# Kernel optimization log

Hardware: AMD Instinct MI355X
Metric: run time of the kernel (lower is better)

The kernel has to match this reference:

```python
import jax, jax.numpy as jnp
import numpy as np

N = 20000      # nodes
E = 640000     # edges (before self loops)
IN = 256       # in_channels == out_channels (forced by classifier size 4*in)
H1, C1 = 8, 16   # conv1: heads=8, out=16 -> concat 128
H2, C2 = 1, 256  # conv2: heads=1, out=out_channels
B = 4096       # article pairs
NEG_SLOPE = 0.2  # PyG GATv2Conv default negative_slope


def setup_inputs() -> dict:
    key = jax.random.key(0)
    ks = jax.random.split(key, 24)
    s = 0.05
    inp = {
        "gnn_x": jax.random.normal(ks[0], (N, IN), jnp.float32),
        "vanilla_x": jax.random.normal(ks[1], (N, IN), jnp.float32),
        "edge_src": jax.random.randint(ks[2], (E,), 0, N, jnp.int32),
        "edge_dst": jax.random.randint(ks[3], (E,), 0, N, jnp.int32),
        "a1_idx": jax.random.randint(ks[4], (B,), 0, N, jnp.int64),
        "a2_idx": jax.random.randint(ks[5], (B,), 0, N, jnp.int64),
        # conv1 params (lin_l, lin_r, att, bias)
        "Wl1": jax.random.normal(ks[6], (IN, H1 * C1), jnp.float32) * s,
        "bl1": jnp.zeros((H1 * C1,), jnp.float32),
        "Wr1": jax.random.normal(ks[7], (IN, H1 * C1), jnp.float32) * s,
        "br1": jnp.zeros((H1 * C1,), jnp.float32),
        "att1": jax.random.normal(ks[8], (H1, C1), jnp.float32) * s,
        "bias1": jnp.zeros((H1 * C1,), jnp.float32),
        # conv2 params
        "Wl2": jax.random.normal(ks[9], (H1 * C1, H2 * C2), jnp.float32) * s,
        "bl2": jnp.zeros((H2 * C2,), jnp.float32),
        "Wr2": jax.random.normal(ks[10], (H1 * C1, H2 * C2), jnp.float32) * s,
        "br2": jnp.zeros((H2 * C2,), jnp.float32),
        "att2": jax.random.normal(ks[11], (H2, C2), jnp.float32) * s,
        "bias2": jnp.zeros((H2 * C2,), jnp.float32),
        # classifier
        "Wc": jax.random.normal(ks[12], (4 * IN, 1), jnp.float32) * s,
        "bc": jnp.zeros((1,), jnp.float32),
    }
    return inp


def _gatv2_layer(x, src, dst, Wl, bl, Wr, br, att, bias):
    """GATv2Conv: x_l = lin_l(x)[src], x_r = lin_r(x)[dst];
    e = att . leaky_relu(x_l + x_r); segment softmax over dst; scatter-add x_l*alpha."""
    n = x.shape[0]
    h, c = att.shape
    xl = (x @ Wl + bl).reshape(n, h, c)
    xr = (x @ Wr + br).reshape(n, h, c)
    # per-edge attention logits [E, H]
    e = jnp.einsum('ehc,hc->eh', jax.nn.leaky_relu(xl[src] + xr[dst], NEG_SLOPE), att)
    # segment softmax over destination nodes (self loops guarantee non-empty segments)
    emax = jax.ops.segment_max(e, dst, num_segments=n)
    ex = jnp.exp(e - emax[dst])
    denom = jax.ops.segment_sum(ex, dst, num_segments=n)
    alpha = ex / denom[dst]                      # [E, H]
    out = jax.ops.segment_sum(alpha[:, :, None] * xl[src], dst, num_segments=n)  # [N,H,C]
    return out.reshape(n, h * c) + bias          # concat=True (heads=1 identical)


def reference(gnn_x, vanilla_x, Wl1, bl1, Wr1, br1, att1, bias1,
              Wl2, bl2, Wr2, br2, att2, bias2, Wc, bc,
              edge_src, edge_dst, a1_idx, a2_idx):
    n = gnn_x.shape[0]
    loops = jnp.arange(n, dtype=edge_src.dtype)
    src = jnp.concatenate([edge_src, loops])     # PyG add_self_loops=True
    dst = jnp.concatenate([edge_dst, loops])
    x = _gatv2_layer(gnn_x, src, dst, Wl1, bl1, Wr1, br1, att1, bias1)
    x = jax.nn.relu(x)
    x = _gatv2_layer(x, src, dst, Wl2, bl2, Wr2, br2, att2, bias2)
    combined = jnp.concatenate(
        [vanilla_x[a1_idx], vanilla_x[a2_idx], x[a1_idx], x[a2_idx]], axis=1)  # [B, 4*IN]
    logits = combined @ Wc + bc                  # [B, 1]
    return logits
```

## Files before the change

### kernel.cpp

```cpp
#include <hip/hip_runtime.h>
#include <math.h>

#define N_NODES 20000
#define M_PAD   20032
#define E_EDGES 640000
#define ET (E_EDGES + N_NODES)
#define IN_CH 256
#define D1 128
#define D2 256
#define BPAIRS 4096
#define NEG 0.2f
#define LOG2E 1.4426950408889634f

#define ZC_BLOCKS    40
#define WT_BLOCKS    32
#define XCONV_BLOCKS (M_PAD * IN_CH / 4 / 4 / 256)
#define PREP_BLOCKS  (ZC_BLOCKS + WT_BLOCKS + XCONV_BLOCKS)

#define COUNT_BLOCKS ((ET + 255) / 256)
#define SCAT_BLOCKS  ((ET + 255) / 256)
#define G1X (M_PAD / 64)
#define G1_BLOCKS (G1X * (D1 / 64))
#define K2_GEMM0 (1 + COUNT_BLOCKS)
#define K2_SCAT0 (K2_GEMM0 + G1_BLOCKS)
#define K2_BLOCKS (K2_SCAT0 + SCAT_BLOCKS)

#if __has_builtin(__builtin_amdgcn_exp2f)
#define EXP2F(x) __builtin_amdgcn_exp2f(x)
#else
#define EXP2F(x) exp2f(x)
#endif

typedef __bf16 bf16x8 __attribute__((ext_vector_type(8)));
typedef float  f32x4  __attribute__((ext_vector_type(4)));
typedef float  f32x2  __attribute__((ext_vector_type(2)));
typedef unsigned short u16x4 __attribute__((ext_vector_type(4)));

__device__ __forceinline__ unsigned short f2b(float f) {
    unsigned int u = __float_as_uint(f);
    unsigned int r = u + 0x7FFFu + ((u >> 16) & 1u);
    return (unsigned short)(r >> 16);
}
__device__ __forceinline__ unsigned char f2f8(float f) {
    return (unsigned char)(__builtin_amdgcn_cvt_pk_fp8_f32(f, f, 0, false) & 0xFF);
}
template <bool HI>
__device__ __forceinline__ f32x2 f8up2(unsigned int u) {
    return __builtin_amdgcn_cvt_pk_f32_fp8((int)u, HI);
}
__device__ __forceinline__ f32x2 up2(unsigned int u) {
    f32x2 r;
    r.x = __uint_as_float(u << 16);
    r.y = __uint_as_float(u & 0xFFFF0000u);
    return r;
}
__device__ __forceinline__ f32x2 lrelu2(f32x2 s) {
    return __builtin_elementwise_max(s, s * NEG);
}
__device__ __forceinline__ float lrelu(float s) { return fmaxf(s, NEG * s); }

__device__ __forceinline__ void unpack8(uint4 u, float* v) {
    v[0] = __uint_as_float(u.x << 16); v[1] = __uint_as_float(u.x & 0xFFFF0000u);
    v[2] = __uint_as_float(u.y << 16); v[3] = __uint_as_float(u.y & 0xFFFF0000u);
    v[4] = __uint_as_float(u.z << 16); v[5] = __uint_as_float(u.z & 0xFFFF0000u);
    v[6] = __uint_as_float(u.w << 16); v[7] = __uint_as_float(u.w & 0xFFFF0000u);
}
__device__ __forceinline__ void unpack8_f8(uint2 u, float* v) {
    f32x2 a = f8up2<false>(u.x), b = f8up2<true>(u.x);
    f32x2 c = f8up2<false>(u.y), d = f8up2<true>(u.y);
    v[0] = a.x; v[1] = a.y; v[2] = b.x; v[3] = b.y;
    v[4] = c.x; v[5] = c.y; v[6] = d.x; v[7] = d.y;
}

__device__ __forceinline__ int aload(const int* p) {
    return __hip_atomic_load(p, __ATOMIC_RELAXED, __HIP_MEMORY_SCOPE_AGENT);
}


__global__ __launch_bounds__(256) void prep_kernel(
        const float* __restrict__ gnn_x,
        const float* __restrict__ Wl1, const float* __restrict__ Wr1,
        const float* __restrict__ Wl2, const float* __restrict__ Wr2,
        unsigned short* __restrict__ xb,
        unsigned short* __restrict__ wt1l, unsigned short* __restrict__ wt1r,
        unsigned short* __restrict__ wt2l, unsigned short* __restrict__ wt2r,
        int* __restrict__ ibuf) {
    __shared__ __align__(16) unsigned short tile[64 * 65];
    int bid = blockIdx.x;
    if (bid < ZC_BLOCKS) {
        int q = bid * 256 + threadIdx.x;
        int4 z; z.x = z.y = z.z = z.w = 0;
        ((int4*)ibuf)[q] = z;
    } else if (bid < ZC_BLOCKS + WT_BLOCKS) {
        int t = bid - ZC_BLOCKS;
        int m = t >> 3;
        int tt = t & 7;
        const float* W;
        unsigned short* Wt;
        int K, N;
        if (m == 0)      { W = Wl1; Wt = wt1l; K = IN_CH; N = D1; }
        else if (m == 1) { W = Wr1; Wt = wt1r; K = IN_CH; N = D1; }
        else if (m == 2) { W = Wl2; Wt = wt2l; K = D1; N = D2; }
        else             { W = Wr2; Wt = wt2r; K = D1; N = D2; }
        int ntn = N >> 6;
        int k0 = (tt / ntn) << 6;
        int n0 = (tt % ntn) << 6;
        int c = threadIdx.x & 63;
        int rr = threadIdx.x >> 6;
#pragma unroll
        for (int ch = 0; ch < 16; ch++) {
            int row = rr * 16 + ch;
            tile[row * 65 + c] = f2b(W[(size_t)(k0 + row) * N + n0 + c]);
        }
        __syncthreads();
#pragma unroll
        for (int ch = 0; ch < 16; ch++) {
            int n = rr * 16 + ch;
            Wt[(size_t)(n0 + n) * K + k0 + c] = tile[c * 65 + n];
        }
    } else {
        int tid = (bid - ZC_BLOCKS - WT_BLOCKS) * 256 + threadIdx.x;
        const int NQ = M_PAD * IN_CH / 4;
        int q0 = tid * 4;
#pragma unroll
        for (int j = 0; j < 4; j++) {
            int qi = q0 + j;
            if (qi >= NQ) break;
            int e0 = qi * 4;
            int row = e0 >> 8;
            u16x4 o;
            if (row < N_NODES) {
                f32x4 v = __builtin_nontemporal_load((const f32x4*)(gnn_x + e0));
                o.x = f2b(v.x); o.y = f2b(v.y); o.z = f2b(v.z); o.w = f2b(v.w);
            } else {
                o.x = o.y = o.z = o.w = 0;
            }
            *(u16x4*)(xb + e0) = o;
        }
    }
}

__device__ __forceinline__ void scan256(const int* __restrict__ count,
                                        int* __restrict__ offsets,
                                        int* wbuf) {
    const int PER = 79;
    int t = threadIdx.x;
    int base = t * PER;
    int sum = 0;
#pragma unroll 8
    for (int i = 0; i < PER; i++) {
        int idx = base + i;
        if (idx < N_NODES) sum += count[idx];
    }
    int lane = t & 63, wave = t >> 6;
    int s = sum;
#pragma unroll
    for (int off = 1; off < 64; off <<= 1) {
        int x = __shfl_up(s, off);
        if (lane >= off) s += x;
    }
    int* wsum = wbuf;
    int* wpre = wbuf + 4;
    if (lane == 63) wsum[wave] = s;
    __syncthreads();
    if (t == 0) {
        int acc = 0;
        for (int w = 0; w < 4; w++) { wpre[w] = acc; acc += wsum[w]; }
    }
    __syncthreads();
    int excl = wpre[wave] + (s - sum);
    if (t == 255) offsets[N_NODES] = excl + sum;
    int run = excl;
#pragma unroll 8
    for (int i = 0; i < PER; i++) {
        int idx = base + i;
        if (idx < N_NODES) { offsets[idx] = run; run += count[idx]; }
    }
}

template <int K>
__device__ __forceinline__ void dual_gemm_tile(
        const unsigned short* __restrict__ A,
        const unsigned short* __restrict__ Wtl,
        const unsigned short* __restrict__ Wtr,
        const float* __restrict__ bl, const float* __restrict__ br,
        unsigned char* __restrict__ Yl, unsigned short* __restrict__ Yr,
        int M, int NOUT, int bx, int by) {
    const int NK = K / 32;
    int wave = threadIdx.x >> 6;
    int lane = threadIdx.x & 63;
    int row0 = bx * 64;
    int col0 = (by * 4 + wave) * 16;
    int rsub = lane & 15;
    int koff = (lane >> 4) * 8;

    const unsigned short* ap  = A   + (size_t)(row0 + rsub) * K + koff;
    const unsigned short* bpl = Wtl + (size_t)(col0 + rsub) * K + koff;
    const unsigned short* bpr = Wtr + (size_t)(col0 + rsub) * K + koff;

    f32x4 l0 = {0.f, 0.f, 0.f, 0.f};
    f32x4 l1 = l0, l2 = l0, l3 = l0, r0 = l0, r1 = l0, r2 = l0, r3 = l0;

#pragma unroll
    for (int kb = 0; kb < NK; kb++) {
        int off = kb * 32;
        bf16x8 bfl = *(const bf16x8*)(bpl + off);
        bf16x8 bfr = *(const bf16x8*)(bpr + off);
        bf16x8 a0 = *(const bf16x8*)(ap + off);
        bf16x8 a1 = *(const bf16x8*)(ap + 16 * K + off);
        bf16x8 a2 = *(const bf16x8*)(ap + 32 * K + off);
        bf16x8 a3 = *(const bf16x8*)(ap + 48 * K + off);
        l0 = __builtin_amdgcn_mfma_f32_16x16x32_bf16(a0, bfl, l0, 0, 0, 0);
        r0 = __builtin_amdgcn_mfma_f32_16x16x32_bf16(a0, bfr, r0, 0, 0, 0);
        l1 = __builtin_amdgcn_mfma_f32_16x16x32_bf16(a1, bfl, l1, 0, 0, 0);
        r1 = __builtin_amdgcn_mfma_f32_16x16x32_bf16(a1, bfr, r1, 0, 0, 0);
        l2 = __builtin_amdgcn_mfma_f32_16x16x32_bf16(a2, bfl, l2, 0, 0, 0);
        r2 = __builtin_amdgcn_mfma_f32_16x16x32_bf16(a2, bfr, r2, 0, 0, 0);
        l3 = __builtin_amdgcn_mfma_f32_16x16x32_bf16(a3, bfl, l3, 0, 0, 0);
        r3 = __builtin_amdgcn_mfma_f32_16x16x32_bf16(a3, bfr, r3, 0, 0, 0);
    }

    int colg = col0 + rsub;
    float bvl = bl[colg];
    float bvr = br[colg];
    int rbase = row0 + (lane >> 4) * 4;
#pragma unroll
    for (int t = 0; t < 4; t++) {
        f32x4 al = (t == 0) ? l0 : (t == 1) ? l1 : (t == 2) ? l2 : l3;
        f32x4 ar = (t == 0) ? r0 : (t == 1) ? r1 : (t == 2) ? r2 : r3;
#pragma unroll
        for (int r = 0; r < 4; r++) {
            int row = rbase + t * 16 + r;
            if (row < M) {
                Yl[(size_t)row * NOUT + colg] = f2f8(al[r] + bvl);
                Yr[(size_t)row * NOUT + colg] = f2b(ar[r] + bvr);
            }
        }
    }
}


__global__ __launch_bounds__(256) void sort_gemm1_kernel(
        const int* __restrict__ edge_src, const int* __restrict__ edge_dst,
        int* __restrict__ count, int* __restrict__ cursor,
        int* __restrict__ done, int* __restrict__ flag,
        int* __restrict__ offsets, int* __restrict__ sorted_src,
        const unsigned short* __restrict__ A,
        const unsigned short* __restrict__ Wtl,
        const unsigned short* __restrict__ Wtr,
        const float* __restrict__ bl, const float* __restrict__ br,
        unsigned char* __restrict__ Yl, unsigned short* __restrict__ Yr) {
    __shared__ int wbuf[8];
    int bid = blockIdx.x, tid = threadIdx.x;
    if (bid == 0) {
        if (tid == 0) {
            int guard = 0;
            while (aload(done) < COUNT_BLOCKS && guard < (1 << 30)) {
                __builtin_amdgcn_s_sleep(8); guard++;
            }
        }
        __syncthreads();
        scan256(count, offsets, wbuf);
        __builtin_amdgcn_s_waitcnt(0);
        __syncthreads();
        if (tid == 0)
            __hip_atomic_store(flag, 1, __ATOMIC_RELEASE,
                               __HIP_MEMORY_SCOPE_AGENT);
    } else if (bid <= COUNT_BLOCKS) {
        int e = (bid - 1) * 256 + tid;
        if (e < ET) {
            int dst = (e < E_EDGES) ? edge_dst[e] : (e - E_EDGES);
            atomicAdd(&count[dst], 1);
        }
        __builtin_amdgcn_s_waitcnt(0);
        __syncthreads();
        if (tid == 0)
            __hip_atomic_fetch_add(done, 1, __ATOMIC_RELAXED,
                                   __HIP_MEMORY_SCOPE_AGENT);
    } else if (bid < K2_SCAT0) {
        int t = bid - K2_GEMM0;
        dual_gemm_tile<IN_CH>(A, Wtl, Wtr, bl, br, Yl, Yr,
                              N_NODES, D1, t % G1X, t / G1X);
    } else {
        if (tid == 0) {
            int guard = 0;
            while (aload(flag) == 0 && guard < (1 << 30)) {
                __builtin_amdgcn_s_sleep(8); guard++;
            }
        }
        __syncthreads();
        int e = (bid - K2_SCAT0) * 256 + tid;
        if (e < ET) {
            int dst = (e < E_EDGES) ? edge_dst[e] : (e - E_EDGES);
            int src = (e < E_EDGES) ? edge_src[e] : (e - E_EDGES);
            sorted_src[offsets[dst] + atomicAdd(&cursor[dst], 1)] = src;
        }
    }
}


__global__ __launch_bounds__(256) void aggregate1_kernel(
        const unsigned char* __restrict__ xl1, const unsigned short* __restrict__ xr1,
        const float* __restrict__ att1, const float* __restrict__ bias1,
        const int* __restrict__ offsets, const int* __restrict__ sorted_src,
        unsigned short* __restrict__ x1) {
    int wave = threadIdx.x >> 6;
    int lane = threadIdx.x & 63;
    int q = lane >> 4;
    int ql = lane & 15;
    int dst = blockIdx.x * 4 + wave;
    if (dst >= M_PAD) return;
    int c0 = ql * 8;
    if (dst >= N_NODES) {
        if (q == 0) {
            uint4 z; z.x = z.y = z.z = z.w = 0;
            *(uint4*)(x1 + (size_t)dst * D1 + c0) = z;
        }
        return;
    }

    uint4 xu = *(const uint4*)(xr1 + (size_t)dst * D1 + c0);
    f32x2 xr[4] = {up2(xu.x), up2(xu.y), up2(xu.z), up2(xu.w)};
    float4 aa0 = *(const float4*)(att1 + c0);
    float4 aa1 = *(const float4*)(att1 + c0 + 4);
    f32x2 att[4];
    att[0].x = aa0.x * LOG2E; att[0].y = aa0.y * LOG2E;
    att[1].x = aa0.z * LOG2E; att[1].y = aa0.w * LOG2E;
    att[2].x = aa1.x * LOG2E; att[2].y = aa1.y * LOG2E;
    att[3].x = aa1.z * LOG2E; att[3].y = aa1.w * LOG2E;

    int beg = offsets[dst], end = offsets[dst + 1];
    const unsigned char* base = xl1 + c0;

    float l = 0.f;
    f32x2 acc[4] = {{0.f,0.f},{0.f,0.f},{0.f,0.f},{0.f,0.f}};

    int i = beg;
    int s0 = sorted_src[min(i + q, end - 1)];
    uint2 g0 = *(const uint2*)(base + (size_t)s0 * D1);
    bool more1 = (i + 4) < end;
    uint2 g1;
    if (more1) {
        int s1 = sorted_src[min(i + 4 + q, end - 1)];
        g1 = *(const uint2*)(base + (size_t)s1 * D1);
    }
    while (true) {
        bool more2 = (i + 8) < end;
        uint2 g2;
        if (more2) {
            int s2 = sorted_src[min(i + 8 + q, end - 1)];
            g2 = *(const uint2*)(base + (size_t)s2 * D1);
        }
        bool act = (i + q) < end;
        f32x2 v0 = f8up2<false>(g0.x), v1 = f8up2<true>(g0.x);
        f32x2 v2 = f8up2<false>(g0.y), v3 = f8up2<true>(g0.y);
        f32x2 p2 = att[0] * lrelu2(v0 + xr[0]);
        p2 += att[1] * lrelu2(v1 + xr[1]);
        p2 += att[2] * lrelu2(v2 + xr[2]);
        p2 += att[3] * lrelu2(v3 + xr[3]);
        float p = p2.x + p2.y;
        p += __shfl_xor(p, 1);
        float w = act ? EXP2F(p) : 0.f;
        l += w;
        acc[0] += w * v0; acc[1] += w * v1; acc[2] += w * v2; acc[3] += w * v3;
        if (!more1) break;
        i += 4;
        g0 = g1; g1 = g2; more1 = more2;
    }
    l += __shfl_xor(l, 16);
    l += __shfl_xor(l, 32);
#pragma unroll
    for (int j = 0; j < 4; j++) {
        f32x2 t;
        t.x = __shfl_xor(acc[j].x, 16); t.y = __shfl_xor(acc[j].y, 16);
        acc[j] += t;
        t.x = __shfl_xor(acc[j].x, 32); t.y = __shfl_xor(acc[j].y, 32);
        acc[j] += t;
    }
    if (q == 0) {
        float inv = 1.f / l;
        float4 bb0 = *(const float4*)(bias1 + c0);
        float4 bb1 = *(const float4*)(bias1 + c0 + 4);
        unsigned short o[8];
        o[0] = f2b(fmaxf(acc[0].x * inv + bb0.x, 0.f));
        o[1] = f2b(fmaxf(acc[0].y * inv + bb0.y, 0.f));
        o[2] = f2b(fmaxf(acc[1].x * inv + bb0.z, 0.f));
        o[3] = f2b(fmaxf(acc[1].y * inv + bb0.w, 0.f));
        o[4] = f2b(fmaxf(acc[2].x * inv + bb1.x, 0.f));
        o[5] = f2b(fmaxf(acc[2].y * inv + bb1.y, 0.f));
        o[6] = f2b(fmaxf(acc[3].x * inv + bb1.z, 0.f));
        o[7] = f2b(fmaxf(acc[3].y * inv + bb1.w, 0.f));
        uint4 ov;
        ov.x = (unsigned int)o[0] | ((unsigned int)o[1] << 16);
        ov.y = (unsigned int)o[2] | ((unsigned int)o[3] << 16);
        ov.z = (unsigned int)o[4] | ((unsigned int)o[5] << 16);
        ov.w = (unsigned int)o[6] | ((unsigned int)o[7] << 16);
        *(uint4*)(x1 + (size_t)dst * D1 + c0) = ov;
    }
}


template <int K>
__global__ __launch_bounds__(256) void dual_gemm_w32_kernel(
        const unsigned short* __restrict__ A,
        const unsigned short* __restrict__ Wtl,
        const unsigned short* __restrict__ Wtr,
        const float* __restrict__ bl, const float* __restrict__ br,
        unsigned char* __restrict__ Yl, unsigned short* __restrict__ Yr,
        int M, int NOUT) {
    const int NK = K / 32;
    int wave = threadIdx.x >> 6;
    int lane = threadIdx.x & 63;
    int row0 = blockIdx.x * 64;
    int col0 = blockIdx.y * 128 + wave * 32;
    int rsub = lane & 15;
    int koff = (lane >> 4) * 8;

    const unsigned short* ap = A + (size_t)(row0 + rsub) * K + koff;

    bf16x8 bfl[2][NK], bfr[2][NK];
#pragma unroll
    for (int c = 0; c < 2; c++) {
        const unsigned short* bpl = Wtl + (size_t)(col0 + c * 16 + rsub) * K + koff;
        const unsigned short* bpr = Wtr + (size_t)(col0 + c * 16 + rsub) * K + koff;
#pragma unroll
        for (int kb = 0; kb < NK; kb++) {
            bfl[c][kb] = *(const bf16x8*)(bpl + kb * 32);
            bfr[c][kb] = *(const bf16x8*)(bpr + kb * 32);
        }
    }

    f32x4 accl[2][4], accr[2][4];
#pragma unroll
    for (int c = 0; c < 2; c++)
#pragma unroll
        for (int t = 0; t < 4; t++) {
            accl[c][t] = (f32x4){0.f, 0.f, 0.f, 0.f};
            accr[c][t] = (f32x4){0.f, 0.f, 0.f, 0.f};
        }

#pragma unroll
    for (int kb = 0; kb < NK; kb++) {
        int off = kb * 32;
        bf16x8 a[4];
        a[0] = *(const bf16x8*)(ap + off);
        a[1] = *(const bf16x8*)(ap + 16 * K + off);
        a[2] = *(const bf16x8*)(ap + 32 * K + off);
        a[3] = *(const bf16x8*)(ap + 48 * K + off);
#pragma unroll
        for (int t = 0; t < 4; t++) {
#pragma unroll
            for (int c = 0; c < 2; c++) {
                accl[c][t] = __builtin_amdgcn_mfma_f32_16x16x32_bf16(
                    a[t], bfl[c][kb], accl[c][t], 0, 0, 0);
                accr[c][t] = __builtin_amdgcn_mfma_f32_16x16x32_bf16(
                    a[t], bfr[c][kb], accr[c][t], 0, 0, 0);
            }
        }
    }

    int rbase = row0 + (lane >> 4) * 4;
#pragma unroll
    for (int c = 0; c < 2; c++) {
        int colg = col0 + c * 16 + rsub;
        float bvl = bl[colg];
        float bvr = br[colg];
#pragma unroll
        for (int t = 0; t < 4; t++) {
#pragma unroll
            for (int r = 0; r < 4; r++) {
                int row = rbase + t * 16 + r;
                if (row < M) {
                    Yl[(size_t)row * NOUT + colg] = f2f8(accl[c][t][r] + bvl);
                    Yr[(size_t)row * NOUT + colg] = f2b(accr[c][t][r] + bvr);
                }
            }
        }
    }
}


__global__ __launch_bounds__(256) void agg2_classifier_kernel(
        const unsigned char* __restrict__ xl2, const unsigned short* __restrict__ xr2,
        const float* __restrict__ att2, const float* __restrict__ bias2,
        const int* __restrict__ offsets, const int* __restrict__ sorted_src,
        const float* __restrict__ vanilla_x,
        const int* __restrict__ a1_raw, const int* __restrict__ a2_raw,
        const float* __restrict__ Wc, const float* __restrict__ bc,
        float* __restrict__ out) {
    __shared__ float x2row[2][D2];
    __shared__ float mrg[2][32][9];
    __shared__ float part[4];
    __shared__ int stride_s;
    int t = threadIdx.x;
    if (t < 64) {
        bool z = (t < 31) ? (a1_raw[1 + 2 * t] == 0) : true;
        unsigned long long m = __ballot(z);
        if (t == 0) stride_s = (m == ~0ull) ? 2 : 1;
    }
    __syncthreads();
    int stride = stride_s;
    int b = blockIdx.x;
    int a1 = a1_raw[(long)b * stride];
    int a2 = a2_raw[(long)b * stride];

    int wave = t >> 6;
    int d = wave >> 1;
    int ww = wave & 1;
    int lane = t & 63;
    int half = lane >> 5;
    int hl = lane & 31;
    int c0 = hl * 8;
    int dst = d ? a2 : a1;

    float xr[8], att[8];
    unpack8(*(const uint4*)(xr2 + (size_t)dst * D2 + c0), xr);
#pragma unroll
    for (int j = 0; j < 8; j++) att[j] = att2[c0 + j] * LOG2E;
    int beg = offsets[dst], end = offsets[dst + 1];
    const unsigned char* base = xl2 + c0;

    float l = 0.f;
    float acc[8];
#pragma unroll
    for (int j = 0; j < 8; j++) acc[j] = 0.f;

    int sub = 2 * ww + half;
    int i = beg;
    int s0 = sorted_src[min(i + sub, end - 1)];
    uint2 g0 = *(const uint2*)(base + (size_t)s0 * D2);
    bool more1 = (i + 4) < end;
    uint2 g1;
    if (more1) {
        int s1 = sorted_src[min(i + 4 + sub, end - 1)];
        g1 = *(const uint2*)(base + (size_t)s1 * D2);
    }
    while (true) {
        bool more2 = (i + 8) < end;
        uint2 g2;
        if (more2) {
            int s2 = sorted_src[min(i + 8 + sub, end - 1)];
            g2 = *(const uint2*)(base + (size_t)s2 * D2);
        }
        bool act = (i + sub) < end;
        float v[8];
        unpack8_f8(g0, v);
        float p = 0.f;
#pragma unroll
        for (int j = 0; j < 8; j++) p = fmaf(att[j], lrelu(v[j] + xr[j]), p);
        p += __shfl_xor(p, 1);
        p += __shfl_xor(p, 2);
        p += __shfl_xor(p, 4);
        p += __shfl_xor(p, 8);
        p += __shfl_xor(p, 16);
        float w = act ? EXP2F(p) : 0.f;
        l += w;
#pragma unroll
        for (int j = 0; j < 8; j++) acc[j] += w * v[j];
        if (!more1) break;
        i += 4;
        g0 = g1; g1 = g2; more1 = more2;
    }
    l += __shfl_xor(l, 32);
#pragma unroll
    for (int j = 0; j < 8; j++) acc[j] += __shfl_xor(acc[j], 32);
    if (ww == 1 && half == 0) {
        mrg[d][hl][0] = l;
#pragma unroll
        for (int j = 0; j < 8; j++) mrg[d][hl][1 + j] = acc[j];
    }
    __syncthreads();
    if (ww == 0 && half == 0) {
        l += mrg[d][hl][0];
#pragma unroll
        for (int j = 0; j < 8; j++) acc[j] += mrg[d][hl][1 + j];
        float inv = 1.f / l;
#pragma unroll
        for (int j = 0; j < 8; j++)
            x2row[d][c0 + j] = acc[j] * inv + bias2[c0 + j];
    }
    __syncthreads();

    float s = vanilla_x[(size_t)a1 * IN_CH + t] * Wc[t]
            + vanilla_x[(size_t)a2 * IN_CH + t] * Wc[IN_CH + t]
            + x2row[0][t] * Wc[2 * IN_CH + t]
            + x2row[1][t] * Wc[3 * IN_CH + t];
    s += __shfl_xor(s, 1);
    s += __shfl_xor(s, 2);
    s += __shfl_xor(s, 4);
    s += __shfl_xor(s, 8);
    s += __shfl_xor(s, 16);
    s += __shfl_xor(s, 32);
    if (lane == 0) part[wave] = s;
    __syncthreads();
    if (t == 0) out[b] = part[0] + part[1] + part[2] + part[3] + bc[0];
}


extern "C" void kernel_launch(void* const* d_in, const int* in_sizes, int n_in,
                              void* d_out, int out_size, void* d_ws, size_t ws_size,
                              hipStream_t stream) {
    const float* gnn_x     = (const float*)d_in[0];
    const float* vanilla_x = (const float*)d_in[1];
    const int*   edge_src  = (const int*)d_in[2];
    const int*   edge_dst  = (const int*)d_in[3];
    const int*   a1_idx    = (const int*)d_in[4];
    const int*   a2_idx    = (const int*)d_in[5];
    const float* Wl1   = (const float*)d_in[6];
    const float* bl1   = (const float*)d_in[7];
    const float* Wr1   = (const float*)d_in[8];
    const float* br1   = (const float*)d_in[9];
    const float* att1  = (const float*)d_in[10];
    const float* bias1 = (const float*)d_in[11];
    const float* Wl2   = (const float*)d_in[12];
    const float* bl2   = (const float*)d_in[13];
    const float* Wr2   = (const float*)d_in[14];
    const float* br2   = (const float*)d_in[15];
    const float* att2  = (const float*)d_in[16];
    const float* bias2 = (const float*)d_in[17];
    const float* Wc    = (const float*)d_in[18];
    const float* bc    = (const float*)d_in[19];
    float* out = (float*)d_out;

    char* p = (char*)d_ws;
    unsigned short* xb   = (unsigned short*)p; p += (size_t)M_PAD * IN_CH * 2;
    unsigned short* x1b  = (unsigned short*)p; p += (size_t)M_PAD * D1 * 2;
    unsigned char*  xl1b = (unsigned char*)p;  p += (size_t)N_NODES * D1;
    unsigned short* xr1b = (unsigned short*)p; p += (size_t)N_NODES * D1 * 2;
    unsigned char*  xl2b = (unsigned char*)p;  p += (size_t)N_NODES * D2;
    unsigned short* xr2b = (unsigned short*)p; p += (size_t)N_NODES * D2 * 2;
    unsigned short* wt1l = (unsigned short*)p; p += (size_t)D1 * IN_CH * 2;
    unsigned short* wt1r = (unsigned short*)p; p += (size_t)D1 * IN_CH * 2;
    unsigned short* wt2l = (unsigned short*)p; p += (size_t)D2 * D1 * 2;
    unsigned short* wt2r = (unsigned short*)p; p += (size_t)D2 * D1 * 2;
    int* ibuf       = (int*)p; p += (size_t)40960 * 4;
    int* offsets    = (int*)p; p += (size_t)(N_NODES + 4) * 4;
    int* sorted_src = (int*)p; p += (size_t)ET * 4;
    int* count  = ibuf;
    int* cursor = ibuf + 20032;
    int* done   = ibuf + 40064;
    int* flag   = ibuf + 40128;

    prep_kernel<<<PREP_BLOCKS, 256, 0, stream>>>(
        gnn_x, Wl1, Wr1, Wl2, Wr2, xb, wt1l, wt1r, wt2l, wt2r, ibuf);

    sort_gemm1_kernel<<<K2_BLOCKS, 256, 0, stream>>>(
        edge_src, edge_dst, count, cursor, done, flag, offsets, sorted_src,
        xb, wt1l, wt1r, bl1, br1, xl1b, xr1b);

    aggregate1_kernel<<<M_PAD / 4, 256, 0, stream>>>(
        xl1b, xr1b, att1, bias1, offsets, sorted_src, x1b);

    dim3 g2(M_PAD / 64, D2 / 128);
    dual_gemm_w32_kernel<D1><<<g2, 256, 0, stream>>>(
        x1b, wt2l, wt2r, bl2, br2, xl2b, xr2b, N_NODES, D2);

    agg2_classifier_kernel<<<BPAIRS, 256, 0, stream>>>(
        xl2b, xr2b, att2, bias2, offsets, sorted_src,
        vanilla_x, a1_idx, a2_idx, Wc, bc, out);
}
```

Measured before the change: 314.2 us.

## Split counting/scan into separate kernel using last-block scan, drop spin-wait flags

The fused sort+GEMM kernel used spin-waiting blocks (one scan block waiting on all count blocks, scatter blocks waiting on a flag). It is now split into a count kernel where the last-arriving block does the prefix scan, followed by a kernel that runs the scatter and the layer-1 GEMM tiles together. This removes the in-kernel spin-wait dependencies and the risk of blocks sleeping while holding CU slots, at the cost of one extra launch and losing overlap between counting and the GEMM. The GEMM tile also preloads all weight fragments into registers before the k-loop, which raises register pressure.

```diff
diff --git a/kernel.cpp b/kernel.cpp
--- a/kernel.cpp
+++ b/kernel.cpp
@@ -21,9 +21,7 @@
 #define SCAT_BLOCKS  ((ET + 255) / 256)
 #define G1X (M_PAD / 64)
 #define G1_BLOCKS (G1X * (D1 / 64))
-#define K2_GEMM0 (1 + COUNT_BLOCKS)
-#define K2_SCAT0 (K2_GEMM0 + G1_BLOCKS)
-#define K2_BLOCKS (K2_SCAT0 + SCAT_BLOCKS)
+#define K3_BLOCKS (SCAT_BLOCKS + G1_BLOCKS)
 
 #if __has_builtin(__builtin_amdgcn_exp2f)
 #define EXP2F(x) __builtin_amdgcn_exp2f(x)
@@ -70,10 +68,6 @@
     f32x2 c = f8up2<false>(u.y), d = f8up2<true>(u.y);
     v[0] = a.x; v[1] = a.y; v[2] = b.x; v[3] = b.y;
     v[4] = c.x; v[5] = c.y; v[6] = d.x; v[7] = d.y;
-}
-
-__device__ __forceinline__ int aload(const int* p) {
-    return __hip_atomic_load(p, __ATOMIC_RELAXED, __HIP_MEMORY_SCOPE_AGENT);
 }
 
 
@@ -178,6 +172,33 @@
     }
 }
 
+
+__global__ __launch_bounds__(256) void count_scan_kernel(
+        const int* __restrict__ edge_dst,
+        int* __restrict__ count, int* __restrict__ done,
+        int* __restrict__ offsets) {
+    __shared__ int wbuf[8];
+    __shared__ int islast;
+    int bid = blockIdx.x, tid = threadIdx.x;
+    int e = bid * 256 + tid;
+    if (e < ET) {
+        int dst = (e < E_EDGES) ? edge_dst[e] : (e - E_EDGES);
+        atomicAdd(&count[dst], 1);
+    }
+    __builtin_amdgcn_s_waitcnt(0);
+    __syncthreads();
+    if (tid == 0) {
+        int old = __hip_atomic_fetch_add(done, 1, __ATOMIC_RELAXED,
+                                         __HIP_MEMORY_SCOPE_AGENT);
+        islast = (old == COUNT_BLOCKS - 1) ? 1 : 0;
+    }
+    __syncthreads();
+    if (islast) {
+        scan256(count, offsets, wbuf);
+    }
+}
+
+
 template <int K>
 __device__ __forceinline__ void dual_gemm_tile(
         const unsigned short* __restrict__ A,
@@ -198,26 +219,31 @@
     const unsigned short* bpl = Wtl + (size_t)(col0 + rsub) * K + koff;
     const unsigned short* bpr = Wtr + (size_t)(col0 + rsub) * K + koff;
 
+    bf16x8 bfl[NK], bfr[NK];
+#pragma unroll
+    for (int kb = 0; kb < NK; kb++) {
+        bfl[kb] = *(const bf16x8*)(bpl + kb * 32);
+        bfr[kb] = *(const bf16x8*)(bpr + kb * 32);
+    }
+
     f32x4 l0 = {0.f, 0.f, 0.f, 0.f};
     f32x4 l1 = l0, l2 = l0, l3 = l0, r0 = l0, r1 = l0, r2 = l0, r3 = l0;
 
 #pragma unroll
     for (int kb = 0; kb < NK; kb++) {
         int off = kb * 32;
-        bf16x8 bfl = *(const bf16x8*)(bpl + off);
-        bf16x8 bfr = *(const bf16x8*)(bpr + off);
         bf16x8 a0 = *(const bf16x8*)(ap + off);
         bf16x8 a1 = *(const bf16x8*)(ap + 16 * K + off);
         bf16x8 a2 = *(const bf16x8*)(ap + 32 * K + off);
         bf16x8 a3 = *(const bf16x8*)(ap + 48 * K + off);
-        l0 = __builtin_amdgcn_mfma_f32_16x16x32_bf16(a0, bfl, l0, 0, 0, 0);
-        r0 = __builtin_amdgcn_mfma_f32_16x16x32_bf16(a0, bfr, r0, 0, 0, 0);
-        l1 = __builtin_amdgcn_mfma_f32_16x16x32_bf16(a1, bfl, l1, 0, 0, 0);
-        r1 = __builtin_amdgcn_mfma_f32_16x16x32_bf16(a1, bfr, r1, 0, 0, 0);
-        l2 = __builtin_amdgcn_mfma_f32_16x16x32_bf16(a2, bfl, l2, 0, 0, 0);
-        r2 = __builtin_amdgcn_mfma_f32_16x16x32_bf16(a2, bfr, r2, 0, 0, 0);
-        l3 = __builtin_amdgcn_mfma_f32_16x16x32_bf16(a3, bfl, l3, 0, 0, 0);
-        r3 = __builtin_amdgcn_mfma_f32_16x16x32_bf16(a3, bfr, r3, 0, 0, 0);
+        l0 = __builtin_amdgcn_mfma_f32_16x16x32_bf16(a0, bfl[kb], l0, 0, 0, 0);
+        r0 = __builtin_amdgcn_mfma_f32_16x16x32_bf16(a0, bfr[kb], r0, 0, 0, 0);
+        l1 = __builtin_amdgcn_mfma_f32_16x16x32_bf16(a1, bfl[kb], l1, 0, 0, 0);
+        r1 = __builtin_amdgcn_mfma_f32_16x16x32_bf16(a1, bfr[kb], r1, 0, 0, 0);
+        l2 = __builtin_amdgcn_mfma_f32_16x16x32_bf16(a2, bfl[kb], l2, 0, 0, 0);
+        r2 = __builtin_amdgcn_mfma_f32_16x16x32_bf16(a2, bfr[kb], r2, 0, 0, 0);
+        l3 = __builtin_amdgcn_mfma_f32_16x16x32_bf16(a3, bfl[kb], l3, 0, 0, 0);
+        r3 = __builtin_amdgcn_mfma_f32_16x16x32_bf16(a3, bfr[kb], r3, 0, 0, 0);
     }
 
     int colg = col0 + rsub;
@@ -240,61 +266,26 @@
 }
 
 
-__global__ __launch_bounds__(256) void sort_gemm1_kernel(
+__global__ __launch_bounds__(256) void scat_gemm1_kernel(
         const int* __restrict__ edge_src, const int* __restrict__ edge_dst,
-        int* __restrict__ count, int* __restrict__ cursor,
-        int* __restrict__ done, int* __restrict__ flag,
-        int* __restrict__ offsets, int* __restrict__ sorted_src,
+        const int* __restrict__ offsets, int* __restrict__ cursor,
+        int* __restrict__ sorted_src,
         const unsigned short* __restrict__ A,
         const unsigned short* __restrict__ Wtl,
         const unsigned short* __restrict__ Wtr,
         const float* __restrict__ bl, const float* __restrict__ br,
         unsigned char* __restrict__ Yl, unsigned short* __restrict__ Yr) {
-    __shared__ int wbuf[8];
-    int bid = blockIdx.x, tid = threadIdx.x;
-    if (bid == 0) {
-        if (tid == 0) {
-            int guard = 0;
-            while (aload(done) < COUNT_BLOCKS && guard < (1 << 30)) {
-                __builtin_amdgcn_s_sleep(8); guard++;
-            }
-        }
-        __syncthreads();
-        scan256(count, offsets, wbuf);
-        __builtin_amdgcn_s_waitcnt(0);
-        __syncthreads();
-        if (tid == 0)
-            __hip_atomic_store(flag, 1, __ATOMIC_RELEASE,
-                               __HIP_MEMORY_SCOPE_AGENT);
-    } else if (bid <= COUNT_BLOCKS) {
-        int e = (bid - 1) * 256 + tid;
-        if (e < ET) {
-            int dst = (e < E_EDGES) ? edge_dst[e] : (e - E_EDGES);
-            atomicAdd(&count[dst], 1);
-        }
-        __builtin_amdgcn_s_waitcnt(0);
-        __syncthreads();
-        if (tid == 0)
-            __hip_atomic_fetch_add(done, 1, __ATOMIC_RELAXED,
-                                   __HIP_MEMORY_SCOPE_AGENT);
-    } else if (bid < K2_SCAT0) {
-        int t = bid - K2_GEMM0;
+    int bid = blockIdx.x;
+    if (bid < SCAT_BLOCKS) {
+        int e = bid * 256 + threadIdx.x;
+        if (e >= ET) return;
+        int dst = (e < E_EDGES) ? edge_dst[e] : (e - E_EDGES);
+        int src = (e < E_EDGES) ? edge_src[e] : (e - E_EDGES);
+        sorted_src[offsets[dst] + atomicAdd(&cursor[dst], 1)] = src;
+    } else {
+        int t = bid - SCAT_BLOCKS;
         dual_gemm_tile<IN_CH>(A, Wtl, Wtr, bl, br, Yl, Yr,
                               N_NODES, D1, t % G1X, t / G1X);
-    } else {
-        if (tid == 0) {
-            int guard = 0;
-            while (aload(flag) == 0 && guard < (1 << 30)) {
-                __builtin_amdgcn_s_sleep(8); guard++;
-            }
-        }
-        __syncthreads();
-        int e = (bid - K2_SCAT0) * 256 + tid;
-        if (e < ET) {
-            int dst = (e < E_EDGES) ? edge_dst[e] : (e - E_EDGES);
-            int src = (e < E_EDGES) ? edge_src[e] : (e - E_EDGES);
-            sorted_src[offsets[dst] + atomicAdd(&cursor[dst], 1)] = src;
-        }
     }
 }
 
@@ -639,13 +630,15 @@
     int* count  = ibuf;
     int* cursor = ibuf + 20032;
     int* done   = ibuf + 40064;
-    int* flag   = ibuf + 40128;
 
     prep_kernel<<<PREP_BLOCKS, 256, 0, stream>>>(
         gnn_x, Wl1, Wr1, Wl2, Wr2, xb, wt1l, wt1r, wt2l, wt2r, ibuf);
 
-    sort_gemm1_kernel<<<K2_BLOCKS, 256, 0, stream>>>(
-        edge_src, edge_dst, count, cursor, done, flag, offsets, sorted_src,
+    count_scan_kernel<<<COUNT_BLOCKS, 256, 0, stream>>>(
+        edge_dst, count, done, offsets);
+
+    scat_gemm1_kernel<<<K3_BLOCKS, 256, 0, stream>>>(
+        edge_src, edge_dst, offsets, cursor, sorted_src,
         xb, wt1l, wt1r, bl1, br1, xl1b, xr1b);
 
     aggregate1_kernel<<<M_PAD / 4, 256, 0, stream>>>(
```

After: 325.6 us. 3.6% more time.
